# Kernel optimization log

Hardware: AMD Instinct MI355X
Metric: run time of the kernel (lower is better)

Reference implementation:

```python
import jax, jax.numpy as jnp
import numpy as np

SHAPES = ((100, 100), (50, 50), (25, 25))  # (H, W) per level
B, D, NH, HD, NL, NP, DFF = 4, 256, 8, 32, 3, 4, 1024
L = sum(h * w for h, w in SHAPES)  # 13125
EPS = 1e-5


def _layer_norm(x, g, b):
    m = jnp.mean(x, axis=-1, keepdims=True)
    v = jnp.var(x, axis=-1, keepdims=True)
    return (x - m) * jax.lax.rsqrt(v + EPS) * g + b


def _grid_sample_bilinear(img, grid):
    """img: [N,C,H,W]; grid: [N,Lq,P,2] in [-1,1]; align_corners=False, zero pad.
    Returns [N,C,Lq,P]."""
    N, C, H, W = img.shape
    x = ((grid[..., 0] + 1.0) * W - 1.0) * 0.5
    y = ((grid[..., 1] + 1.0) * H - 1.0) * 0.5
    x0 = jnp.floor(x); y0 = jnp.floor(y)
    x1 = x0 + 1.0; y1 = y0 + 1.0
    wx1 = x - x0; wx0 = 1.0 - wx1
    wy1 = y - y0; wy0 = 1.0 - wy1
    flat = img.reshape(N, C, H * W)

    def gather(ix, iy):
        valid = ((ix >= 0) & (ix < W) & (iy >= 0) & (iy < H)).astype(img.dtype)
        ii = (jnp.clip(iy, 0, H - 1).astype(jnp.int32) * W
              + jnp.clip(ix, 0, W - 1).astype(jnp.int32))  # [N,Lq,P]
        idx = jnp.broadcast_to(ii.reshape(N, 1, -1), (N, C, ii.shape[1] * ii.shape[2]))
        vals = jnp.take_along_axis(flat, idx, axis=2).reshape(N, C, ii.shape[1], ii.shape[2])
        return vals * valid[:, None]

    out = (gather(x0, y0) * (wx0 * wy0)[:, None]
           + gather(x1, y0) * (wx1 * wy0)[:, None]
           + gather(x0, y1) * (wx0 * wy1)[:, None]
           + gather(x1, y1) * (wx1 * wy1)[:, None])
    return out


def _ms_deform_attn_core(value, loc, attn):
    """value: [B,L,NH,HD]; loc: [B,Lq,NH,NL,NP,2] in [0,1]; attn: [B,Lq,NH,NL,NP]."""
    Bn, Lq = loc.shape[0], loc.shape[1]
    grids = 2.0 * loc - 1.0
    start = 0
    samples = []
    for lid, (H, W) in enumerate(SHAPES):
        v = value[:, start:start + H * W]            # [B,HW,NH,HD]
        start += H * W
        v = v.transpose(0, 2, 3, 1).reshape(Bn * NH, HD, H, W)
        g = grids[:, :, :, lid].transpose(0, 2, 1, 3, 4).reshape(Bn * NH, Lq, NP, 2)
        samples.append(_grid_sample_bilinear(v, g))  # [B*NH,HD,Lq,NP]
    sv = jnp.stack(samples, axis=-2).reshape(Bn * NH, HD, Lq, NL * NP)
    a = attn.transpose(0, 2, 1, 3, 4).reshape(Bn * NH, 1, Lq, NL * NP)
    out = (sv * a).sum(-1)                            # [B*NH,HD,Lq]
    return out.reshape(Bn, NH * HD, Lq).transpose(0, 2, 1)


def setup_inputs() -> dict:
    key = jax.random.key(0)
    ks = jax.random.split(key, 16)
    f32 = jnp.float32
    inp = {
        'src': jax.random.normal(ks[0], (B, L, D), f32),
        'pos': jax.random.normal(ks[1], (B, L, D), f32),
        'reference_points': jax.random.uniform(ks[2], (B, L, NL, 2), f32),
        'Wv': jax.random.normal(ks[3], (D, D), f32) * 0.02,
        'bv': jnp.zeros((D,), f32),
        'Woff': jax.random.normal(ks[4], (D, NH * NL * NP * 2), f32) * 0.02,
        'boff': jax.random.normal(ks[5], (NH * NL * NP * 2,), f32) * 0.5,
        'Wattn': jax.random.normal(ks[6], (D, NH * NL * NP), f32) * 0.02,
        'battn': jnp.zeros((NH * NL * NP,), f32),
        'Wout': jax.random.normal(ks[7], (D, D), f32) * 0.02,
        'bout': jnp.zeros((D,), f32),
        'g1': jnp.ones((D,), f32), 'b1': jnp.zeros((D,), f32),
        'Wff1': jax.random.normal(ks[8], (D, DFF), f32) * 0.02,
        'bff1': jnp.zeros((DFF,), f32),
        'Wff2': jax.random.normal(ks[9], (DFF, D), f32) * 0.02,
        'bff2': jnp.zeros((D,), f32),
        'g2': jnp.ones((D,), f32), 'b2': jnp.zeros((D,), f32),
    }
    return inp


def reference(src, pos, reference_points, Wv, bv, Woff, boff, Wattn, battn,
              Wout, bout, g1, b1, Wff1, bff1, Wff2, bff2, g2, b2):
    # DeformableTransformerEncoderLayer forward (eval mode: dropout = identity)
    q = src + pos
    value = (src @ Wv + bv).reshape(B, L, NH, HD)
    off = (q @ Woff + boff).reshape(B, L, NH, NL, NP, 2)
    attn = jax.nn.softmax((q @ Wattn + battn).reshape(B, L, NH, NL * NP), axis=-1)
    attn = attn.reshape(B, L, NH, NL, NP)
    norm = jnp.array([[w, h] for h, w in SHAPES], dtype=src.dtype)  # [NL,2] = (W,H)
    loc = reference_points[:, :, None, :, None, :] + off / norm[None, None, None, :, None, :]
    attn_out = _ms_deform_attn_core(value, loc, attn) @ Wout + bout
    x = _layer_norm(src + attn_out, g1, b1)
    ff = jax.nn.relu(x @ Wff1 + bff1) @ Wff2 + bff2
    return _layer_norm(x + ff, g2, b2)
```

## Files before the change

kernel.cpp:

```cpp
#include <hip/hip_runtime.h>


#define BLTOK 52500
#define MP    52608
#define LSP   13125

using short8  = __attribute__((ext_vector_type(8))) short;
using ushort8v= __attribute__((ext_vector_type(8))) unsigned short;
using f32x4   = __attribute__((ext_vector_type(4))) float;
using fl2     = __attribute__((ext_vector_type(2))) float;

__device__ __forceinline__ ushort f2b(float f) {
  union { float f; unsigned u; } x; x.f = f;
  unsigned r = (x.u + 0x7fffu + ((x.u >> 16) & 1u)) >> 16;
  return (ushort)r;
}
__device__ __forceinline__ float b2f(ushort h) {
  union { unsigned u; float f; } x; x.u = ((unsigned)h) << 16;
  return x.f;
}
__device__ __forceinline__ float blo(uint u) {
  union { unsigned u; float f; } x; x.u = u << 16;
  return x.f;
}
__device__ __forceinline__ float bhi(uint u) {
  union { unsigned u; float f; } x; x.u = u & 0xffff0000u;
  return x.f;
}

#define GLDS16(gp, lp) __builtin_amdgcn_global_load_lds( \
    (const __attribute__((address_space(1))) void*)(gp), \
    (__attribute__((address_space(3))) void*)(lp), 16, 0, 0)

__global__ __launch_bounds__(256) void prep_weights(
    const float* __restrict__ Wv, const float* __restrict__ Woff,
    const float* __restrict__ Wattn, const float* __restrict__ Wout,
    const float* __restrict__ Wff1, const float* __restrict__ Wff2,
    const float* __restrict__ boff, const float* __restrict__ battn,
    ushort* __restrict__ wv_t, ushort* __restrict__ wcat_t,
    ushort* __restrict__ wout_t, ushort* __restrict__ wff1_t,
    ushort* __restrict__ wff2_t, float* __restrict__ bcat)
{
  int i = blockIdx.x * 256 + threadIdx.x;
  if (i < 65536) {
    int n = i >> 8, k = i & 255;
    wv_t[i] = f2b(Wv[k * 256 + n]);
    return;
  }
  int j = i - 65536;
  if (j < 98304) {
    int n = j >> 8, k = j & 255;
    float v = (n < 192) ? Woff[k * 192 + n]
            : (n < 288) ? Wattn[k * 96 + (n - 192)] : 0.f;
    wcat_t[j] = f2b(v);
    return;
  }
  j -= 98304;
  if (j < 65536) {
    int n = j >> 8, k = j & 255;
    wout_t[j] = f2b(Wout[k * 256 + n]);
    return;
  }
  j -= 65536;
  if (j < 262144) {
    int n = j >> 8, k = j & 255;
    wff1_t[j] = f2b(Wff1[k * 1024 + n]);
    return;
  }
  j -= 262144;
  if (j < 262144) {
    int n = j >> 10, k = j & 1023;
    wff2_t[j] = f2b(Wff2[k * 256 + n]);
    return;
  }
  j -= 262144;
  if (j < 384) bcat[j] = (j < 192) ? boff[j] : (j < 288) ? battn[j - 192] : 0.f;
}

__global__ __launch_bounds__(256) void prep_act(
    const float* __restrict__ src, const float* __restrict__ pos,
    ushort* __restrict__ src_bf, ushort* __restrict__ q_bf)
{
  const size_t e = ((size_t)blockIdx.x * 256 + threadIdx.x) * 4;
  if (e >= (size_t)MP * 256) return;
  ushort4 sb, qb;
  if (e < (size_t)BLTOK * 256) {
    const float4 s = *(const float4*)(src + e);
    const float4 p = *(const float4*)(pos + e);
    sb.x = f2b(s.x); sb.y = f2b(s.y); sb.z = f2b(s.z); sb.w = f2b(s.w);
    qb.x = f2b(s.x + p.x); qb.y = f2b(s.y + p.y);
    qb.z = f2b(s.z + p.z); qb.w = f2b(s.w + p.w);
  } else {
    sb.x = sb.y = sb.z = sb.w = 0;
    qb.x = qb.y = qb.z = qb.w = 0;
  }
  *(ushort4*)(src_bf + e) = sb;
  *(ushort4*)(q_bf + e) = qb;
}

template <int EPI>
__global__ __launch_bounds__(256) void gemm128(
    const ushort* __restrict__ A, const ushort* __restrict__ Bt,
    const float* __restrict__ bias, const float* __restrict__ addf,
    const ushort* __restrict__ addb, ushort* __restrict__ C,
    int Mact, int Nact, int Nstr, int K)
{
  __shared__ __align__(16) ushort sm[16384];
  ushort* As = sm;
  ushort* Bs = sm + 8192;
  float*  epf = (float*)sm;
  const int tid = threadIdx.x;
  const int wave = tid >> 6, lane = tid & 63;
  const int n0 = blockIdx.x * 128, m0 = blockIdx.y * 128;
  const int srow = lane >> 2, skc = (lane & 3) * 8;
  const ushort* Ag = A + (size_t)(m0 + wave * 32 + srow) * K + skc;
  const ushort* Bg = Bt + (size_t)(n0 + wave * 32 + srow) * K + skc;
  const int quad = lane >> 4, l16 = lane & 15;
  const int wm = (wave & 1) * 64, wn = (wave >> 1) * 64;
  f32x4 acc[4][4] = {};

#define STAGE(buf, kk) { \
    ushort* la = As + (buf) * 4096 + wave * 1024; \
    ushort* lb = Bs + (buf) * 4096 + wave * 1024; \
    GLDS16(Ag + (kk), la); \
    GLDS16(Ag + (kk) + 16 * K, la + 512); \
    GLDS16(Bg + (kk), lb); \
    GLDS16(Bg + (kk) + 16 * K, lb + 512); }

  STAGE(0, 0);
  int cur = 0;
  for (int k0 = 0; k0 < K; k0 += 32) {
    __syncthreads();
    if (k0 + 32 < K) STAGE(cur ^ 1, k0 + 32);
    const ushort* Ab = As + cur * 4096;
    const ushort* Bb = Bs + cur * 4096;
    short8 af[4], bf[4];
#pragma unroll
    for (int i = 0; i < 4; i++)
      af[i] = *(const short8*)(&Ab[(wm + i * 16 + l16) * 32 + quad * 8]);
#pragma unroll
    for (int j = 0; j < 4; j++)
      bf[j] = *(const short8*)(&Bb[(wn + j * 16 + l16) * 32 + quad * 8]);
#pragma unroll
    for (int i = 0; i < 4; i++)
#pragma unroll
      for (int j = 0; j < 4; j++)
        acc[i][j] = __builtin_amdgcn_mfma_f32_16x16x32_bf16(af[i], bf[j],
                                                            acc[i][j], 0, 0, 0);
    cur ^= 1;
  }
#undef STAGE

  for (int half = 0; half < 2; half++) {
    __syncthreads();
    if ((wave & 1) == half) {
#pragma unroll
      for (int i = 0; i < 4; i++)
#pragma unroll
        for (int j = 0; j < 4; j++)
#pragma unroll
          for (int r = 0; r < 4; r++)
            epf[(i * 16 + quad * 4 + r) * 128 + wn + j * 16 + l16] = acc[i][j][r];
    }
    __syncthreads();
    const int gm0 = m0 + half * 64;
#pragma unroll
    for (int g = 0; g < 4; g++) {
      const int lrow = g * 16 + (tid >> 4);
      const int col0 = (tid & 15) * 8;
      const int grow = gm0 + lrow;
      const int gcol = n0 + col0;
      if (grow < Mact && gcol < Nact) {
        float v[8];
#pragma unroll
        for (int c = 0; c < 8; c++) v[c] = epf[lrow * 128 + col0 + c] + bias[gcol + c];
        const size_t idx = (size_t)grow * Nstr + gcol;
        if (EPI == 1) {
          const float4 a0 = *(const float4*)(addf + idx);
          const float4 a1 = *(const float4*)(addf + idx + 4);
          v[0] += a0.x; v[1] += a0.y; v[2] += a0.z; v[3] += a0.w;
          v[4] += a1.x; v[5] += a1.y; v[6] += a1.z; v[7] += a1.w;
        }
        if (EPI == 2) {
#pragma unroll
          for (int c = 0; c < 8; c++) v[c] = fmaxf(v[c], 0.f);
        }
        if (EPI == 3) {
          const ushort8v ab = *(const ushort8v*)(addb + idx);
#pragma unroll
          for (int c = 0; c < 8; c++) v[c] += b2f(ab[c]);
        }
        ushort8v o;
#pragma unroll
        for (int c = 0; c < 8; c++) o[c] = f2b(v[c]);
        *(ushort8v*)(C + idx) = o;
      }
    }
  }
}

__global__ __launch_bounds__(256) void deform_sample(
    const ushort* __restrict__ value, const ushort* __restrict__ oa_all,
    const float* __restrict__ refp, ushort* __restrict__ outb)
{
  const int tid = threadIdx.x;
  const int xcd  = blockIdx.x & 7;
  const int slot = blockIdx.x >> 3;
  const int batch = xcd >> 1, halfb = xcd & 1;
  const int tok = batch * LSP + halfb * 6564 + slot * 8 + (tid >> 5);
  const int tokEnd = batch * LSP + (halfb ? LSP : 6564);
  if (tok >= tokEnd) return;
  const int l = tid & 31;
  const int h = l >> 2;
  const int q = l & 3;
  const ushort* oa = oa_all + (uint)tok * 320u;
  const float* rp = refp + (uint)tok * 6u;
  const uint base = (uint)batch * (LSP * 256u) + (uint)(l * 8);

  const int Wl[3] = {100, 50, 25};
  const int Stl[3] = {0, 10000, 12500};

  const ushort* lgp = oa + 192 + h * 12 + q;
  float e0 = b2f(lgp[0]), e1 = b2f(lgp[4]), e2 = b2f(lgp[8]);
  float m3 = fmaxf(fmaxf(e0, e1), e2);
  m3 = fmaxf(m3, __shfl_xor(m3, 1, 4));
  m3 = fmaxf(m3, __shfl_xor(m3, 2, 4));
  e0 = __expf(e0 - m3); e1 = __expf(e1 - m3); e2 = __expf(e2 - m3);
  float s3 = e0 + e1 + e2;
  s3 += __shfl_xor(s3, 1, 4);
  s3 += __shfl_xor(s3, 2, 4);
  const float inv = __builtin_amdgcn_rcpf(s3);
  const float awn[3] = {e0 * inv, e1 * inv, e2 * inv};

  float ow[3][4];
  uint  orr[3][4];
#pragma unroll
  for (int lid = 0; lid < 3; lid++) {
    const int W = Wl[lid], st = Stl[lid];
    const float Wf = (float)W;
    const uint o = *(const uint*)(oa + h * 24 + lid * 8 + q * 2);
    const float aw = awn[lid];
    const float x = rp[lid * 2] * Wf - 0.5f + blo(o);
    const float y = rp[lid * 2 + 1] * Wf - 0.5f + bhi(o);
    const float x0f = floorf(x), y0f = floorf(y);
    const float wx1 = x - x0f, wy1 = y - y0f;
    const float wx0 = 1.f - wx1, wy0 = 1.f - wy1;
    const int ix0 = (int)x0f, iy0 = (int)y0f;
    const bool x0v = (ix0 >= 0) & (ix0 < W);
    const bool x1v = (ix0 + 1 >= 0) & (ix0 + 1 < W);
    const bool y0v = (iy0 >= 0) & (iy0 < W);
    const bool y1v = (iy0 + 1 >= 0) & (iy0 + 1 < W);
    const float ay0 = aw * wy0, ay1 = aw * wy1;
    ow[lid][0] = (x0v & y0v) ? ay0 * wx0 : 0.f;
    ow[lid][1] = (x1v & y0v) ? ay0 * wx1 : 0.f;
    ow[lid][2] = (x0v & y1v) ? ay1 * wx0 : 0.f;
    ow[lid][3] = (x1v & y1v) ? ay1 * wx1 : 0.f;
    const int ix0c = min(max(ix0, 0), W - 1);
    const int ix1c = min(max(ix0 + 1, 0), W - 1);
    const int iy0c = min(max(iy0, 0), W - 1);
    const int iy1c = min(max(iy0 + 1, 0), W - 1);
    orr[lid][0] = (uint)(st + iy0c * W + ix0c) * 256u;
    orr[lid][1] = (uint)(st + iy0c * W + ix1c) * 256u;
    orr[lid][2] = (uint)(st + iy1c * W + ix0c) * 256u;
    orr[lid][3] = (uint)(st + iy1c * W + ix1c) * 256u;
  }

  fl2 acc2[4] = {};
#pragma unroll
  for (int lid = 0; lid < 3; lid++) {
    float bw[4][4];
    uint4 cq[4][4];
#pragma unroll
    for (int pt = 0; pt < 4; pt++) {
#pragma unroll
      for (int c = 0; c < 4; c++) {
        bw[pt][c] = __shfl(ow[lid][c], pt, 4);
        const uint r = (uint)__shfl((int)orr[lid][c], pt, 4);
        cq[pt][c] = *(const uint4*)(value + base + r);
      }
    }
    __builtin_amdgcn_sched_barrier(0);
#pragma unroll
    for (int pt = 0; pt < 4; pt++) {
#pragma unroll
      for (int c = 0; c < 4; c++) {
        const fl2 wv = {bw[pt][c], bw[pt][c]};
        const uint* u = (const uint*)&cq[pt][c];
#pragma unroll
        for (int pp = 0; pp < 4; pp++) {
          const fl2 vv = {blo(u[pp]), bhi(u[pp])};
          acc2[pp] += wv * vv;
        }
      }
    }
  }

  ushort4 o0, o1;
  o0.x = f2b(acc2[0].x); o0.y = f2b(acc2[0].y);
  o0.z = f2b(acc2[1].x); o0.w = f2b(acc2[1].y);
  o1.x = f2b(acc2[2].x); o1.y = f2b(acc2[2].y);
  o1.z = f2b(acc2[3].x); o1.w = f2b(acc2[3].y);
  ushort* op = outb + (uint)tok * 256u + (uint)(l * 8);
  *(ushort4*)op = o0;
  *(ushort4*)(op + 4) = o1;
}

template <int OUTF>
__global__ __launch_bounds__(256) void ln256(
    const ushort* __restrict__ in, const float* __restrict__ gg,
    const float* __restrict__ bb, ushort* __restrict__ outb,
    float* __restrict__ outf, int rows)
{
  const int wave = threadIdx.x >> 6, lane = threadIdx.x & 63;
  const int r = blockIdx.x * 4 + wave;
  if (r >= rows) return;
  const ushort* rowp = in + (size_t)r * 256;
  const ushort4 u = *(const ushort4*)(rowp + lane * 4);
  float v[4] = {b2f(u.x), b2f(u.y), b2f(u.z), b2f(u.w)};
  float s = v[0] + v[1] + v[2] + v[3];
  float s2 = v[0] * v[0] + v[1] * v[1] + v[2] * v[2] + v[3] * v[3];
#pragma unroll
  for (int o = 32; o > 0; o >>= 1) {
    s += __shfl_xor(s, o);
    s2 += __shfl_xor(s2, o);
  }
  const float mean = s * (1.f / 256.f);
  const float var = s2 * (1.f / 256.f) - mean * mean;
  const float rstd = rsqrtf(var + 1e-5f);
#pragma unroll
  for (int j = 0; j < 4; j++) {
    const int col = lane * 4 + j;
    const float o = (v[j] - mean) * rstd * gg[col] + bb[col];
    if (OUTF) outf[(size_t)r * 256 + col] = o;
    else outb[(size_t)r * 256 + col] = f2b(o);
  }
}

extern "C" void kernel_launch(void* const* d_in, const int* in_sizes, int n_in,
                              void* d_out, int out_size, void* d_ws, size_t ws_size,
                              hipStream_t stream)
{
  const float* src   = (const float*)d_in[0];
  const float* pos   = (const float*)d_in[1];
  const float* refp  = (const float*)d_in[2];
  const float* Wv    = (const float*)d_in[3];
  const float* bv    = (const float*)d_in[4];
  const float* Woff  = (const float*)d_in[5];
  const float* boff  = (const float*)d_in[6];
  const float* Wattn = (const float*)d_in[7];
  const float* battn = (const float*)d_in[8];
  const float* Wout  = (const float*)d_in[9];
  const float* bout  = (const float*)d_in[10];
  const float* g1    = (const float*)d_in[11];
  const float* b1    = (const float*)d_in[12];
  const float* Wff1  = (const float*)d_in[13];
  const float* bff1  = (const float*)d_in[14];
  const float* Wff2  = (const float*)d_in[15];
  const float* bff2  = (const float*)d_in[16];
  const float* g2    = (const float*)d_in[17];
  const float* b2    = (const float*)d_in[18];
  float* out = (float*)d_out;
  char* ws = (char*)d_ws;

  ushort* wcat_t = (ushort*)(ws + 0);
  ushort* wff1_t = (ushort*)(ws + 196608);
  ushort* wff2_t = (ushort*)(ws + 720896);
  float*  bcat   = (float*)(ws + 1245184);
  ushort* A1 = (ushort*)(ws + 1246720);
  ushort* A2 = (ushort*)(ws + 28182016);
  ushort* A3 = (ushort*)(ws + 55117312);
  ushort* A4 = (ushort*)(ws + 81997312);
  ushort* A5 = (ushort*)(ws + 115597312);
  ushort* wout_t = (ushort*)(ws + 223076352);
  ushort* wv_t   = (ushort*)(ws + 223207424);

  prep_weights<<<2946, 256, 0, stream>>>(Wv, Woff, Wattn, Wout, Wff1, Wff2,
                                         boff, battn,
                                         wv_t, wcat_t, wout_t, wff1_t, wff2_t, bcat);
  prep_act<<<MP / 4, 256, 0, stream>>>(src, pos, A1, A2);
  gemm128<0><<<dim3(2, MP / 128), 256, 0, stream>>>(A1, wv_t, bv, nullptr, nullptr,
                                                    A3, BLTOK, 256, 256, 256);
  gemm128<0><<<dim3(3, MP / 128), 256, 0, stream>>>(A2, wcat_t, bcat, nullptr, nullptr,
                                                    A4, BLTOK, 320, 320, 256);
  deform_sample<<<8 * 821, 256, 0, stream>>>(A3, A4, refp, A5);
  gemm128<3><<<dim3(2, MP / 128), 256, 0, stream>>>(A5, wout_t, bout, nullptr, A1,
                                                    A4, BLTOK, 256, 256, 256);
  ln256<0><<<BLTOK / 4, 256, 0, stream>>>(A4, g1, b1, A2, nullptr, BLTOK);
  gemm128<2><<<dim3(8, MP / 128), 256, 0, stream>>>(A2, wff1_t, bff1, nullptr, nullptr,
                                                    A5, MP, 1024, 1024, 256);
  gemm128<3><<<dim3(2, MP / 128), 256, 0, stream>>>(A5, wff2_t, bff2, nullptr, A2,
                                                    A3, BLTOK, 256, 256, 1024);
  ln256<1><<<BLTOK / 4, 256, 0, stream>>>(A3, g2, b2, nullptr, out, BLTOK);
}
```

Measured before the change: 469.3 us.

## Fuse residual-add and LayerNorm into full-row output GEMM; persistent deform sampler

```diff
diff --git a/kernel.cpp b/kernel.cpp
--- a/kernel.cpp
+++ b/kernel.cpp
@@ -101,8 +101,7 @@
 template <int EPI>
 __global__ __launch_bounds__(256) void gemm128(
     const ushort* __restrict__ A, const ushort* __restrict__ Bt,
-    const float* __restrict__ bias, const float* __restrict__ addf,
-    const ushort* __restrict__ addb, ushort* __restrict__ C,
+    const float* __restrict__ bias, ushort* __restrict__ C,
     int Mact, int Nact, int Nstr, int K)
 {
   __shared__ __align__(16) ushort sm[16384];
@@ -174,26 +173,137 @@
         float v[8];
 #pragma unroll
         for (int c = 0; c < 8; c++) v[c] = epf[lrow * 128 + col0 + c] + bias[gcol + c];
-        const size_t idx = (size_t)grow * Nstr + gcol;
-        if (EPI == 1) {
-          const float4 a0 = *(const float4*)(addf + idx);
-          const float4 a1 = *(const float4*)(addf + idx + 4);
-          v[0] += a0.x; v[1] += a0.y; v[2] += a0.z; v[3] += a0.w;
-          v[4] += a1.x; v[5] += a1.y; v[6] += a1.z; v[7] += a1.w;
-        }
         if (EPI == 2) {
 #pragma unroll
           for (int c = 0; c < 8; c++) v[c] = fmaxf(v[c], 0.f);
         }
-        if (EPI == 3) {
-          const ushort8v ab = *(const ushort8v*)(addb + idx);
-#pragma unroll
-          for (int c = 0; c < 8; c++) v[c] += b2f(ab[c]);
+        ushort8v o;
+#pragma unroll
+        for (int c = 0; c < 8; c++) o[c] = f2b(v[c]);
+        *(ushort8v*)(C + (size_t)grow * Nstr + gcol) = o;
+      }
+    }
+  }
+}
+
+template <int OUTF>
+__global__ __launch_bounds__(512) void gemm_ln(
+    const ushort* __restrict__ A, const ushort* __restrict__ Bt,
+    const float* __restrict__ bias, const ushort* __restrict__ addb,
+    const float* __restrict__ gg, const float* __restrict__ bb,
+    ushort* __restrict__ outb, float* __restrict__ outf, int K)
+{
+  __shared__ __align__(16) ushort sm[24576];
+  ushort* As = sm;
+  ushort* Bs = sm + 8192;
+  float*  epf = (float*)sm;
+  const int tid = threadIdx.x;
+  const int w = tid >> 6, lane = tid & 63;
+  const int m0 = blockIdx.x * 128;
+  const int srow = lane >> 2, skc = (lane & 3) * 8;
+  const ushort* Ag = A + (size_t)(m0 + w * 16 + srow) * K + skc;
+  const ushort* Bg = Bt + (size_t)(w * 32 + srow) * K + skc;
+  const int quad = lane >> 4, l16 = lane & 15;
+  const int wm = (w & 1) * 64, wn = (w >> 1) * 64;
+  f32x4 acc[4][4] = {};
+
+#define STAGE8(buf, kk) { \
+    ushort* la = As + (buf) * 4096 + w * 512; \
+    ushort* lb = Bs + (buf) * 8192 + w * 1024; \
+    GLDS16(Ag + (kk), la); \
+    GLDS16(Bg + (kk), lb); \
+    GLDS16(Bg + (kk) + 16 * K, lb + 512); }
+
+  STAGE8(0, 0);
+  int cur = 0;
+  for (int k0 = 0; k0 < K; k0 += 32) {
+    __syncthreads();
+    if (k0 + 32 < K) STAGE8(cur ^ 1, k0 + 32);
+    const ushort* Ab = As + cur * 4096;
+    const ushort* Bb = Bs + cur * 8192;
+    short8 af[4], bf[4];
+#pragma unroll
+    for (int i = 0; i < 4; i++)
+      af[i] = *(const short8*)(&Ab[(wm + i * 16 + l16) * 32 + quad * 8]);
+#pragma unroll
+    for (int j = 0; j < 4; j++)
+      bf[j] = *(const short8*)(&Bb[(wn + j * 16 + l16) * 32 + quad * 8]);
+#pragma unroll
+    for (int i = 0; i < 4; i++)
+#pragma unroll
+      for (int j = 0; j < 4; j++)
+        acc[i][j] = __builtin_amdgcn_mfma_f32_16x16x32_bf16(af[i], bf[j],
+                                                            acc[i][j], 0, 0, 0);
+    cur ^= 1;
+  }
+#undef STAGE8
+
+  const int r2 = tid >> 4;
+  const int cb = tid & 15;
+#pragma unroll
+  for (int q = 0; q < 4; q++) {
+    __syncthreads();
+    if ((w & 1) == (q >> 1)) {
+#pragma unroll
+      for (int i2 = 0; i2 < 2; i2++) {
+        const int i = (q & 1) * 2 + i2;
+        const int lr = i2 * 16 + quad * 4;
+#pragma unroll
+        for (int j = 0; j < 4; j++)
+#pragma unroll
+          for (int r = 0; r < 4; r++)
+            epf[(lr + r) * 258 + wn + j * 16 + l16] = acc[i][j][r];
+      }
+    }
+    __syncthreads();
+    const int grow = m0 + q * 32 + r2;
+    const bool live = (grow < BLTOK);
+    float v[16];
+#pragma unroll
+    for (int ch = 0; ch < 4; ch++) {
+      const int c0 = ch * 64 + cb * 4;
+      const fl2 a = *(const fl2*)(&epf[r2 * 258 + c0]);
+      const fl2 b = *(const fl2*)(&epf[r2 * 258 + c0 + 2]);
+      v[ch * 4 + 0] = a.x; v[ch * 4 + 1] = a.y;
+      v[ch * 4 + 2] = b.x; v[ch * 4 + 3] = b.y;
+      if (live) {
+        const float4 bi = *(const float4*)(bias + c0);
+        const ushort4 ad = *(const ushort4*)(addb + (size_t)grow * 256 + c0);
+        v[ch * 4 + 0] += bi.x + b2f(ad.x);
+        v[ch * 4 + 1] += bi.y + b2f(ad.y);
+        v[ch * 4 + 2] += bi.z + b2f(ad.z);
+        v[ch * 4 + 3] += bi.w + b2f(ad.w);
+      }
+    }
+    float s = 0.f, s2 = 0.f;
+#pragma unroll
+    for (int k = 0; k < 16; k++) { s += v[k]; s2 += v[k] * v[k]; }
+#pragma unroll
+    for (int o = 8; o > 0; o >>= 1) {
+      s += __shfl_xor(s, o, 16);
+      s2 += __shfl_xor(s2, o, 16);
+    }
+    const float mean = s * (1.f / 256.f);
+    const float var = s2 * (1.f / 256.f) - mean * mean;
+    const float rstd = rsqrtf(var + 1e-5f);
+    if (live) {
+#pragma unroll
+      for (int ch = 0; ch < 4; ch++) {
+        const int c0 = ch * 64 + cb * 4;
+        const float4 g4 = *(const float4*)(gg + c0);
+        const float4 b4 = *(const float4*)(bb + c0);
+        float o0 = (v[ch * 4 + 0] - mean) * rstd * g4.x + b4.x;
+        float o1 = (v[ch * 4 + 1] - mean) * rstd * g4.y + b4.y;
+        float o2 = (v[ch * 4 + 2] - mean) * rstd * g4.z + b4.z;
+        float o3 = (v[ch * 4 + 3] - mean) * rstd * g4.w + b4.w;
+        if (OUTF) {
+          float4 o; o.x = o0; o.y = o1; o.z = o2; o.w = o3;
+          *(float4*)(outf + (size_t)grow * 256 + c0) = o;
+        } else {
+          ushort4 o;
+          o.x = f2b(o0); o.y = f2b(o1); o.z = f2b(o2); o.w = f2b(o3);
+          *(ushort4*)(outb + (size_t)grow * 256 + c0) = o;
         }
-        ushort8v o;
-#pragma unroll
-        for (int c = 0; c < 8; c++) o[c] = f2b(v[c]);
-        *(ushort8v*)(C + idx) = o;
       }
     }
   }
@@ -205,134 +315,105 @@
 {
   const int tid = threadIdx.x;
   const int xcd  = blockIdx.x & 7;
-  const int slot = blockIdx.x >> 3;
   const int batch = xcd >> 1, halfb = xcd & 1;
-  const int tok = batch * LSP + halfb * 6564 + slot * 8 + (tid >> 5);
+  const int tokBase = batch * LSP + halfb * 6564;
   const int tokEnd = batch * LSP + (halfb ? LSP : 6564);
-  if (tok >= tokEnd) return;
+  const int Wl[3] = {100, 50, 25};
+  const int Stl[3] = {0, 10000, 12500};
   const int l = tid & 31;
   const int h = l >> 2;
   const int q = l & 3;
-  const ushort* oa = oa_all + (uint)tok * 320u;
-  const float* rp = refp + (uint)tok * 6u;
-  const uint base = (uint)batch * (LSP * 256u) + (uint)(l * 8);
-
-  const int Wl[3] = {100, 50, 25};
-  const int Stl[3] = {0, 10000, 12500};
-
-  const ushort* lgp = oa + 192 + h * 12 + q;
-  float e0 = b2f(lgp[0]), e1 = b2f(lgp[4]), e2 = b2f(lgp[8]);
-  float m3 = fmaxf(fmaxf(e0, e1), e2);
-  m3 = fmaxf(m3, __shfl_xor(m3, 1, 4));
-  m3 = fmaxf(m3, __shfl_xor(m3, 2, 4));
-  e0 = __expf(e0 - m3); e1 = __expf(e1 - m3); e2 = __expf(e2 - m3);
-  float s3 = e0 + e1 + e2;
-  s3 += __shfl_xor(s3, 1, 4);
-  s3 += __shfl_xor(s3, 2, 4);
-  const float inv = __builtin_amdgcn_rcpf(s3);
-  const float awn[3] = {e0 * inv, e1 * inv, e2 * inv};
-
-  float ow[3][4];
-  uint  orr[3][4];
-#pragma unroll
-  for (int lid = 0; lid < 3; lid++) {
-    const int W = Wl[lid], st = Stl[lid];
-    const float Wf = (float)W;
-    const uint o = *(const uint*)(oa + h * 24 + lid * 8 + q * 2);
-    const float aw = awn[lid];
-    const float x = rp[lid * 2] * Wf - 0.5f + blo(o);
-    const float y = rp[lid * 2 + 1] * Wf - 0.5f + bhi(o);
-    const float x0f = floorf(x), y0f = floorf(y);
-    const float wx1 = x - x0f, wy1 = y - y0f;
-    const float wx0 = 1.f - wx1, wy0 = 1.f - wy1;
-    const int ix0 = (int)x0f, iy0 = (int)y0f;
-    const bool x0v = (ix0 >= 0) & (ix0 < W);
-    const bool x1v = (ix0 + 1 >= 0) & (ix0 + 1 < W);
-    const bool y0v = (iy0 >= 0) & (iy0 < W);
-    const bool y1v = (iy0 + 1 >= 0) & (iy0 + 1 < W);
-    const float ay0 = aw * wy0, ay1 = aw * wy1;
-    ow[lid][0] = (x0v & y0v) ? ay0 * wx0 : 0.f;
-    ow[lid][1] = (x1v & y0v) ? ay0 * wx1 : 0.f;
-    ow[lid][2] = (x0v & y1v) ? ay1 * wx0 : 0.f;
-    ow[lid][3] = (x1v & y1v) ? ay1 * wx1 : 0.f;
-    const int ix0c = min(max(ix0, 0), W - 1);
-    const int ix1c = min(max(ix0 + 1, 0), W - 1);
-    const int iy0c = min(max(iy0, 0), W - 1);
-    const int iy1c = min(max(iy0 + 1, 0), W - 1);
-    orr[lid][0] = (uint)(st + iy0c * W + ix0c) * 256u;
-    orr[lid][1] = (uint)(st + iy0c * W + ix1c) * 256u;
-    orr[lid][2] = (uint)(st + iy1c * W + ix0c) * 256u;
-    orr[lid][3] = (uint)(st + iy1c * W + ix1c) * 256u;
-  }
-
-  fl2 acc2[4] = {};
-#pragma unroll
-  for (int lid = 0; lid < 3; lid++) {
-    float bw[4][4];
-    uint4 cq[4][4];
-#pragma unroll
-    for (int pt = 0; pt < 4; pt++) {
-#pragma unroll
-      for (int c = 0; c < 4; c++) {
-        bw[pt][c] = __shfl(ow[lid][c], pt, 4);
-        const uint r = (uint)__shfl((int)orr[lid][c], pt, 4);
-        cq[pt][c] = *(const uint4*)(value + base + r);
-      }
-    }
-    __builtin_amdgcn_sched_barrier(0);
-#pragma unroll
-    for (int pt = 0; pt < 4; pt++) {
-#pragma unroll
-      for (int c = 0; c < 4; c++) {
-        const fl2 wv = {bw[pt][c], bw[pt][c]};
-        const uint* u = (const uint*)&cq[pt][c];
-#pragma unroll
-        for (int pp = 0; pp < 4; pp++) {
-          const fl2 vv = {blo(u[pp]), bhi(u[pp])};
-          acc2[pp] += wv * vv;
+
+  for (int slot = blockIdx.x >> 3; slot < 821; slot += 256) {
+    const int tok = tokBase + slot * 8 + (tid >> 5);
+    if (tok >= tokEnd) continue;
+    const ushort* oa = oa_all + (uint)tok * 320u;
+    const float* rp = refp + (uint)tok * 6u;
+    const uint base = (uint)batch * (LSP * 256u) + (uint)(l * 8);
+
+    const ushort* lgp = oa + 192 + h * 12 + q;
+    float e0 = b2f(lgp[0]), e1 = b2f(lgp[4]), e2 = b2f(lgp[8]);
+    float m3 = fmaxf(fmaxf(e0, e1), e2);
+    m3 = fmaxf(m3, __shfl_xor(m3, 1, 4));
+    m3 = fmaxf(m3, __shfl_xor(m3, 2, 4));
+    e0 = __expf(e0 - m3); e1 = __expf(e1 - m3); e2 = __expf(e2 - m3);
+    float s3 = e0 + e1 + e2;
+    s3 += __shfl_xor(s3, 1, 4);
+    s3 += __shfl_xor(s3, 2, 4);
+    const float inv = __builtin_amdgcn_rcpf(s3);
+    const float awn[3] = {e0 * inv, e1 * inv, e2 * inv};
+
+    float ow[3][4];
+    uint  orr[3][4];
+#pragma unroll
+    for (int lid = 0; lid < 3; lid++) {
+      const int W = Wl[lid], st = Stl[lid];
+      const float Wf = (float)W;
+      const uint o = *(const uint*)(oa + h * 24 + lid * 8 + q * 2);
+      const float aw = awn[lid];
+      const float x = rp[lid * 2] * Wf - 0.5f + blo(o);
+      const float y = rp[lid * 2 + 1] * Wf - 0.5f + bhi(o);
+      const float x0f = floorf(x), y0f = floorf(y);
+      const float wx1 = x - x0f, wy1 = y - y0f;
+      const float wx0 = 1.f - wx1, wy0 = 1.f - wy1;
+      const int ix0 = (int)x0f, iy0 = (int)y0f;
+      const bool x0v = (ix0 >= 0) & (ix0 < W);
+      const bool x1v = (ix0 + 1 >= 0) & (ix0 + 1 < W);
+      const bool y0v = (iy0 >= 0) & (iy0 < W);
+      const bool y1v = (iy0 + 1 >= 0) & (iy0 + 1 < W);
+      const float ay0 = aw * wy0, ay1 = aw * wy1;
+      ow[lid][0] = (x0v & y0v) ? ay0 * wx0 : 0.f;
+      ow[lid][1] = (x1v & y0v) ? ay0 * wx1 : 0.f;
+      ow[lid][2] = (x0v & y1v) ? ay1 * wx0 : 0.f;
+      ow[lid][3] = (x1v & y1v) ? ay1 * wx1 : 0.f;
+      const int ix0c = min(max(ix0, 0), W - 1);
+      const int ix1c = min(max(ix0 + 1, 0), W - 1);
+      const int iy0c = min(max(iy0, 0), W - 1);
+      const int iy1c = min(max(iy0 + 1, 0), W - 1);
+      orr[lid][0] = (uint)(st + iy0c * W + ix0c) * 256u;
+      orr[lid][1] = (uint)(st + iy0c * W + ix1c) * 256u;
+      orr[lid][2] = (uint)(st + iy1c * W + ix0c) * 256u;
+      orr[lid][3] = (uint)(st + iy1c * W + ix1c) * 256u;
+    }
+
+    fl2 acc2[4] = {};
+#pragma unroll
+    for (int lid = 0; lid < 3; lid++) {
+      float bw[4][4];
+      uint4 cq[4][4];
+#pragma unroll
+      for (int pt = 0; pt < 4; pt++) {
+#pragma unroll
+        for (int c = 0; c < 4; c++) {
+          bw[pt][c] = __shfl(ow[lid][c], pt, 4);
+          const uint r = (uint)__shfl((int)orr[lid][c], pt, 4);
+          cq[pt][c] = *(const uint4*)(value + base + r);
         }
       }
-    }
-  }
-
-  ushort4 o0, o1;
-  o0.x = f2b(acc2[0].x); o0.y = f2b(acc2[0].y);
-  o0.z = f2b(acc2[1].x); o0.w = f2b(acc2[1].y);
-  o1.x = f2b(acc2[2].x); o1.y = f2b(acc2[2].y);
-  o1.z = f2b(acc2[3].x); o1.w = f2b(acc2[3].y);
-  ushort* op = outb + (uint)tok * 256u + (uint)(l * 8);
-  *(ushort4*)op = o0;
-  *(ushort4*)(op + 4) = o1;
-}
-
-template <int OUTF>
-__global__ __launch_bounds__(256) void ln256(
-    const ushort* __restrict__ in, const float* __restrict__ gg,
-    const float* __restrict__ bb, ushort* __restrict__ outb,
-    float* __restrict__ outf, int rows)
-{
-  const int wave = threadIdx.x >> 6, lane = threadIdx.x & 63;
-  const int r = blockIdx.x * 4 + wave;
-  if (r >= rows) return;
-  const ushort* rowp = in + (size_t)r * 256;
-  const ushort4 u = *(const ushort4*)(rowp + lane * 4);
-  float v[4] = {b2f(u.x), b2f(u.y), b2f(u.z), b2f(u.w)};
-  float s = v[0] + v[1] + v[2] + v[3];
-  float s2 = v[0] * v[0] + v[1] * v[1] + v[2] * v[2] + v[3] * v[3];
-#pragma unroll
-  for (int o = 32; o > 0; o >>= 1) {
-    s += __shfl_xor(s, o);
-    s2 += __shfl_xor(s2, o);
-  }
-  const float mean = s * (1.f / 256.f);
-  const float var = s2 * (1.f / 256.f) - mean * mean;
-  const float rstd = rsqrtf(var + 1e-5f);
-#pragma unroll
-  for (int j = 0; j < 4; j++) {
-    const int col = lane * 4 + j;
-    const float o = (v[j] - mean) * rstd * gg[col] + bb[col];
-    if (OUTF) outf[(size_t)r * 256 + col] = o;
-    else outb[(size_t)r * 256 + col] = f2b(o);
+      __builtin_amdgcn_sched_barrier(0);
+#pragma unroll
+      for (int pt = 0; pt < 4; pt++) {
+#pragma unroll
+        for (int c = 0; c < 4; c++) {
+          const fl2 wv = {bw[pt][c], bw[pt][c]};
+          const uint* u = (const uint*)&cq[pt][c];
+#pragma unroll
+          for (int pp = 0; pp < 4; pp++) {
+            const fl2 vv = {blo(u[pp]), bhi(u[pp])};
+            acc2[pp] += wv * vv;
+          }
+        }
+      }
+    }
+
+    ushort4 o0, o1;
+    o0.x = f2b(acc2[0].x); o0.y = f2b(acc2[0].y);
+    o0.z = f2b(acc2[1].x); o0.w = f2b(acc2[1].y);
+    o1.x = f2b(acc2[2].x); o1.y = f2b(acc2[2].y);
+    o1.z = f2b(acc2[3].x); o1.w = f2b(acc2[3].y);
+    ushort* op = outb + (uint)tok * 256u + (uint)(l * 8);
+    *(ushort4*)op = o0;
+    *(ushort4*)(op + 4) = o1;
   }
 }
 
@@ -378,17 +459,15 @@
                                          boff, battn,
                                          wv_t, wcat_t, wout_t, wff1_t, wff2_t, bcat);
   prep_act<<<MP / 4, 256, 0, stream>>>(src, pos, A1, A2);
-  gemm128<0><<<dim3(2, MP / 128), 256, 0, stream>>>(A1, wv_t, bv, nullptr, nullptr,
-                                                    A3, BLTOK, 256, 256, 256);
-  gemm128<0><<<dim3(3, MP / 128), 256, 0, stream>>>(A2, wcat_t, bcat, nullptr, nullptr,
-                                                    A4, BLTOK, 320, 320, 256);
-  deform_sample<<<8 * 821, 256, 0, stream>>>(A3, A4, refp, A5);
-  gemm128<3><<<dim3(2, MP / 128), 256, 0, stream>>>(A5, wout_t, bout, nullptr, A1,
-                                                    A4, BLTOK, 256, 256, 256);
-  ln256<0><<<BLTOK / 4, 256, 0, stream>>>(A4, g1, b1, A2, nullptr, BLTOK);
-  gemm128<2><<<dim3(8, MP / 128), 256, 0, stream>>>(A2, wff1_t, bff1, nullptr, nullptr,
-                                                    A5, MP, 1024, 1024, 256);
-  gemm128<3><<<dim3(2, MP / 128), 256, 0, stream>>>(A5, wff2_t, bff2, nullptr, A2,
-                                                    A3, BLTOK, 256, 256, 1024);
-  ln256<1><<<BLTOK / 4, 256, 0, stream>>>(A3, g2, b2, nullptr, out, BLTOK);
-}
+  gemm128<0><<<dim3(2, MP / 128), 256, 0, stream>>>(A1, wv_t, bv, A3,
+                                                    BLTOK, 256, 256, 256);
+  gemm128<0><<<dim3(3, MP / 128), 256, 0, stream>>>(A2, wcat_t, bcat, A4,
+                                                    BLTOK, 320, 320, 256);
+  deform_sample<<<2048, 256, 0, stream>>>(A3, A4, refp, A5);
+  gemm_ln<0><<<MP / 128, 512, 0, stream>>>(A5, wout_t, bout, A1, g1, b1,
+                                           A2, nullptr, 256);
+  gemm128<2><<<dim3(8, MP / 128), 256, 0, stream>>>(A2, wff1_t, bff1, A5,
+                                                    MP, 1024, 1024, 256);
+  gemm_ln<1><<<MP / 128, 512, 0, stream>>>(A5, wff2_t, bff2, A2, g2, b2,
+                                           nullptr, out, 1024);
+}
```

Result: faster. 432.1 us (-7.9%).
